# Performance work log

Measured on AMD Instinct MI355X. Metric: run time of the kernel, lower is better.

Reference implementation:

```python
import jax, jax.numpy as jnp
import numpy as np

SEQ_LEN, INPUT_DIM, HIDDEN_DIM, OUTPUT_DIM = 1024, 128, 256, 128
BATCH = 256


def setup_inputs() -> dict:
    key = jax.random.key(0)
    ks = jax.random.split(key, 7)
    s_ih = 1.0 / np.sqrt(INPUT_DIM)
    s_hh = 1.0 / np.sqrt(HIDDEN_DIM)
    return {
        "x": jax.random.normal(ks[0], (BATCH, SEQ_LEN, INPUT_DIM), jnp.float32),
        "W_ih": jax.random.normal(ks[1], (INPUT_DIM, 4 * HIDDEN_DIM), jnp.float32) * s_ih,
        "W_hh": jax.random.normal(ks[2], (HIDDEN_DIM, 4 * HIDDEN_DIM), jnp.float32) * s_hh,
        "b_ih": jax.random.normal(ks[3], (4 * HIDDEN_DIM,), jnp.float32) * s_hh,
        "b_hh": jax.random.normal(ks[4], (4 * HIDDEN_DIM,), jnp.float32) * s_hh,
        "W_out": jax.random.normal(ks[5], (HIDDEN_DIM, OUTPUT_DIM), jnp.float32) * s_hh,
        "b_out": jax.random.normal(ks[6], (OUTPUT_DIM,), jnp.float32) * s_hh,
    }


def reference(x, W_ih, W_hh, b_ih, b_hh, W_out, b_out):
    B, T, _ = x.shape
    H = W_hh.shape[0]
    # Precompute input projections for all timesteps: [T, B, 4H]
    x_proj = jnp.einsum("bti,ig->tbg", x, W_ih) + (b_ih + b_hh)

    def step(carry, xp_t):
        h, c = carry
        gates = xp_t + h @ W_hh  # [B, 4H]
        i_t, f_t, g_t, o_t = jnp.split(gates, 4, axis=1)
        i_t = jax.nn.sigmoid(i_t)
        f_t = jax.nn.sigmoid(f_t)
        g_t = jnp.tanh(g_t)
        o_t = jax.nn.sigmoid(o_t)
        c = f_t * c + i_t * g_t
        h = o_t * jnp.tanh(c)
        return (h, c), None

    h0 = jnp.zeros((B, H), x.dtype)
    c0 = jnp.zeros((B, H), x.dtype)
    (h_T, _), _ = jax.lax.scan(step, (h0, c0), x_proj)
    return h_T @ W_out + b_out
```

## Files before the change

kernel.cpp:

```cpp
#include <hip/hip_runtime.h>
#include <cstdint>


#define T_    1024
#define I_    128
#define H_    256

typedef short s8v __attribute__((ext_vector_type(8)));
typedef float f4v __attribute__((ext_vector_type(4)));
typedef unsigned short u16;
typedef unsigned int   u32;
typedef unsigned long long u64;

__device__ __forceinline__ u16 f2bf(float f) {
  union { float f; u32 u; } v; v.f = f;
  u32 r = v.u + 0x7FFFu + ((v.u >> 16) & 1u);
  return (u16)(r >> 16);
}
__device__ __forceinline__ float bf2f(u16 h) {
  union { u32 u; float f; } v; v.u = ((u32)h) << 16;
  return v.f;
}
__device__ __forceinline__ float sig_(float x)  { return 1.0f / (1.0f + __expf(-x)); }
__device__ __forceinline__ float tanh_(float x) { return 2.0f / (1.0f + __expf(-2.0f * x)) - 1.0f; }

__device__ __forceinline__ void unpack8(const u64 w[4], s8v& hi, s8v& lo) {
  #pragma unroll
  for (int j = 0; j < 4; j++) {
    u32 a = (u32)w[j], b = (u32)(w[j] >> 32);
    hi[2*j]   = (short)(u16)a;        lo[2*j]   = (short)(u16)(a >> 16);
    hi[2*j+1] = (short)(u16)b;        lo[2*j+1] = (short)(u16)(b >> 16);
  }
}

__global__ __launch_bounds__(256, 1) void lstm_persist(
    const float* __restrict__ x, const float* __restrict__ Wih,
    const float* __restrict__ Whh, const float* __restrict__ bih,
    const float* __restrict__ bhh, const float* __restrict__ Wout,
    const float* __restrict__ bout, float* __restrict__ out,
    u32* __restrict__ flags, u32* __restrict__ hbuf)
{
  const int bid  = blockIdx.x;
  const int xcd  = bid & 7;
  const int slot = bid >> 3;
  const int ct   = slot & 15;
  const int g    = ((slot >> 4) << 3) | xcd;
  const int tid  = threadIdx.x;
  const int wave = tid >> 6;
  const int lane = tid & 63;
  const int lm   = lane & 15;
  const int lq   = lane >> 4;

  __shared__ u16   Wlds[2][64][392];
  __shared__ u16   xlds[2][2][16][136];
  __shared__ float partial[4][4][16][20];

  for (int it = tid; it < 384 * 64; it += 256) {
    int k = it >> 6;
    int c = it & 63;
    int gcol = (c >> 4) * 256 + ct * 16 + (c & 15);
    float w = (k < 128) ? Wih[k * 1024 + gcol] : Whh[(k - 128) * 1024 + gcol];
    u16 hi = f2bf(w);
    Wlds[0][c][k] = hi;
    Wlds[1][c][k] = f2bf(w - bf2f(hi));
  }
  __syncthreads();

  s8v wfrag[3][4][2];
  #pragma unroll
  for (int ki = 0; ki < 3; ki++) {
    const int kt = wave + 4 * ki;
    #pragma unroll
    for (int gg = 0; gg < 4; gg++) {
      #pragma unroll
      for (int p = 0; p < 2; p++)
        wfrag[ki][gg][p] = *(const s8v*)&Wlds[p][gg * 16 + lm][kt * 32 + lq * 8];
    }
  }
  __syncthreads();

  const int cm  = tid >> 4;
  const int chc = tid & 15;
  float biasv[4];
  #pragma unroll
  for (int gg = 0; gg < 4; gg++) {
    int col = gg * 256 + ct * 16 + chc;
    biasv[gg] = bih[col] + bhh[col];
  }
  float cstate = 0.0f;

  const int xr  = tid >> 4;
  const int xc0 = (tid & 15) * 8;
  const float* xbase = x + (size_t)(g * 16 + xr) * (T_ * I_) + xc0;

  u32* gflags = flags + g * 32;
  const size_t hpar   = (size_t)16 * 16 * 256;
  const size_t hgbase = (size_t)g * 16 * 256;

  const int pl   = lane & 3;
  u32* fpeer = gflags + (2 * wave + (pl & 1) + 8 * (pl >> 1));

  auto xstore = [&](int par, float4 a, float4 b) {
    float v[8] = {a.x, a.y, a.z, a.w, b.x, b.y, b.z, b.w};
    union { u16 u[8]; s8v s; } hi, lo;
    #pragma unroll
    for (int j = 0; j < 8; j++) {
      u16 h = f2bf(v[j]);
      hi.u[j] = h;
      lo.u[j] = f2bf(v[j] - bf2f(h));
    }
    *(s8v*)&xlds[par][0][xr][xc0] = hi.s;
    *(s8v*)&xlds[par][1][xr][xc0] = lo.s;
  };

  {
    float4 a = *(const float4*)(xbase + 0);
    float4 b = *(const float4*)(xbase + 4);
    xstore(0, a, b);
  }
  __syncthreads();

  for (int t = 0; t < T_; t++) {
    const int par = t & 1;
    const int pn  = (t + 1) & 1;

    const int tn = (t + 1 < T_) ? (t + 1) : t;
    float4 xa = *(const float4*)(xbase + (size_t)tn * I_);
    float4 xb = *(const float4*)(xbase + (size_t)tn * I_ + 4);

    f4v acc[4];
    #pragma unroll
    for (int gg = 0; gg < 4; gg++)
      #pragma unroll
      for (int r = 0; r < 4; r++) acc[gg][r] = 0.0f;

    {
      s8v axh = *(const s8v*)&xlds[par][0][lm][wave * 32 + lq * 8];
      s8v axl = *(const s8v*)&xlds[par][1][lm][wave * 32 + lq * 8];
      #pragma unroll
      for (int gg = 0; gg < 4; gg++) {
        acc[gg] = __builtin_amdgcn_mfma_f32_16x16x32_bf16(axh, wfrag[0][gg][0], acc[gg], 0, 0, 0);
        acc[gg] = __builtin_amdgcn_mfma_f32_16x16x32_bf16(axl, wfrag[0][gg][0], acc[gg], 0, 0, 0);
        acc[gg] = __builtin_amdgcn_mfma_f32_16x16x32_bf16(axh, wfrag[0][gg][1], acc[gg], 0, 0, 0);
      }
    }

    if (t > 0) {
      const u32 s = (u32)t;
      while (true) {
        u32 f = __hip_atomic_load(fpeer, __ATOMIC_RELAXED, __HIP_MEMORY_SCOPE_AGENT);
        if (__all((int)((f - s) <= 1u))) break;
        __builtin_amdgcn_s_sleep(1);
      }
      asm volatile("" ::: "memory");

      const u32* hb0 = hbuf + (size_t)par * hpar + hgbase;
      #pragma unroll
      for (int ki = 1; ki < 3; ki++) {
        const int hk = wave * 32 + (ki - 1) * 128 + lq * 8;
        const u64* hp = (const u64*)(hb0 + (size_t)lm * 256 + hk);
        u64 w[4];
        #pragma unroll
        for (int j = 0; j < 4; j++)
          w[j] = __hip_atomic_load(hp + j, __ATOMIC_RELAXED, __HIP_MEMORY_SCOPE_AGENT);
        s8v ahh, ahl;
        unpack8(w, ahh, ahl);
        #pragma unroll
        for (int gg = 0; gg < 4; gg++) {
          acc[gg] = __builtin_amdgcn_mfma_f32_16x16x32_bf16(ahh, wfrag[ki][gg][0], acc[gg], 0, 0, 0);
          acc[gg] = __builtin_amdgcn_mfma_f32_16x16x32_bf16(ahl, wfrag[ki][gg][0], acc[gg], 0, 0, 0);
          acc[gg] = __builtin_amdgcn_mfma_f32_16x16x32_bf16(ahh, wfrag[ki][gg][1], acc[gg], 0, 0, 0);
        }
      }
    }

    #pragma unroll
    for (int gg = 0; gg < 4; gg++)
      #pragma unroll
      for (int r = 0; r < 4; r++)
        partial[wave][gg][lq * 4 + r][lm] = acc[gg][r];
    __syncthreads();

    float ga = biasv[0], gb = biasv[1], gc = biasv[2], gd = biasv[3];
    #pragma unroll
    for (int w = 0; w < 4; w++) {
      ga += partial[w][0][cm][chc];
      gb += partial[w][1][cm][chc];
      gc += partial[w][2][cm][chc];
      gd += partial[w][3][cm][chc];
    }
    float i_t = sig_(ga), f_t = sig_(gb), g_t = tanh_(gc), o_t = sig_(gd);
    cstate = f_t * cstate + i_t * g_t;
    float h = o_t * tanh_(cstate);

    u16 hhi = f2bf(h);
    u16 hlo = f2bf(h - bf2f(hhi));
    u32 pk  = ((u32)hlo << 16) | (u32)hhi;
    u32* hw = hbuf + (size_t)pn * hpar + hgbase + (size_t)cm * 256 + ct * 16 + chc;
    __hip_atomic_store(hw, pk, __ATOMIC_RELAXED, __HIP_MEMORY_SCOPE_AGENT);

    __syncthreads();
    if (tid == 0)
      __hip_atomic_store(gflags + ct, (u32)(t + 1), __ATOMIC_RELAXED, __HIP_MEMORY_SCOPE_AGENT);

    xstore(pn, xa, xb);
    __syncthreads();
  }

  {
    const u32 s = (u32)T_;
    u32* fp = gflags + lm;
    while (true) {
      u32 f = __hip_atomic_load(fp, __ATOMIC_RELAXED, __HIP_MEMORY_SCOPE_AGENT);
      if (__all((int)((f - s) <= 1u))) break;
      __builtin_amdgcn_s_sleep(1);
    }
    asm volatile("" ::: "memory");
  }
  __syncthreads();
  for (int it = tid; it < 16 * 256; it += 256) {
    int n = it >> 8;
    int k = it & 255;
    float w = (n < 8) ? Wout[k * 128 + ct * 8 + n] : 0.0f;
    u16 hi = f2bf(w);
    Wlds[0][n][k] = hi;
    Wlds[1][n][k] = f2bf(w - bf2f(hi));
  }
  __syncthreads();

  f4v oacc;
  #pragma unroll
  for (int r = 0; r < 4; r++) oacc[r] = 0.0f;
  const u32* hb0 = hbuf + hgbase;
  #pragma unroll
  for (int ki = 0; ki < 2; ki++) {
    const int hk = (wave * 2 + ki) * 32 + lq * 8;
    const u64* hp = (const u64*)(hb0 + (size_t)lm * 256 + hk);
    u64 w[4];
    #pragma unroll
    for (int j = 0; j < 4; j++)
      w[j] = __hip_atomic_load(hp + j, __ATOMIC_RELAXED, __HIP_MEMORY_SCOPE_AGENT);
    s8v ahh, ahl;
    unpack8(w, ahh, ahl);
    s8v bh  = *(const s8v*)&Wlds[0][lm][hk];
    s8v bl  = *(const s8v*)&Wlds[1][lm][hk];
    oacc = __builtin_amdgcn_mfma_f32_16x16x32_bf16(ahh, bh, oacc, 0, 0, 0);
    oacc = __builtin_amdgcn_mfma_f32_16x16x32_bf16(ahl, bh, oacc, 0, 0, 0);
    oacc = __builtin_amdgcn_mfma_f32_16x16x32_bf16(ahh, bl, oacc, 0, 0, 0);
  }
  #pragma unroll
  for (int r = 0; r < 4; r++) partial[wave][0][lq * 4 + r][lm] = oacc[r];
  __syncthreads();

  if (tid < 128) {
    int m  = tid >> 3;
    int oc = tid & 7;
    float v = bout[ct * 8 + oc];
    #pragma unroll
    for (int w = 0; w < 4; w++) v += partial[w][0][m][oc];
    out[(size_t)(g * 16 + m) * 128 + ct * 8 + oc] = v;
  }
}

extern "C" void kernel_launch(void* const* d_in, const int* in_sizes, int n_in,
                              void* d_out, int out_size, void* d_ws, size_t ws_size,
                              hipStream_t stream) {
  const float* x    = (const float*)d_in[0];
  const float* Wih  = (const float*)d_in[1];
  const float* Whh  = (const float*)d_in[2];
  const float* bih  = (const float*)d_in[3];
  const float* bhh  = (const float*)d_in[4];
  const float* Wout = (const float*)d_in[5];
  const float* bout = (const float*)d_in[6];
  float* out = (float*)d_out;

  char* ws = (char*)d_ws;
  u32* flags = (u32*)ws;
  u32* hbuf  = (u32*)(ws + 4096);

  hipLaunchKernelGGL(lstm_persist, dim3(256), dim3(256), 0, stream,
                     x, Wih, Whh, bih, bhh, Wout, bout, out, flags, hbuf);
}
```

Baseline: 3.151 ms.

## Replace per-block step flags with timestep-tagged 64-bit hidden-state words

Drops the separate flag array and the extra barrier plus flag store after each step. Each hidden value is now written as a 64-bit word whose upper half holds the step number, and consumers spin directly on the data until every tag matches. This removes one synchronisation round trip per timestep. In exchange it doubles the hidden-buffer traffic, busy-polls without sleeping, and leaves some dead unpack code.

```diff
diff --git a/kernel.cpp b/kernel.cpp
--- a/kernel.cpp
+++ b/kernel.cpp
@@ -24,12 +24,13 @@
 __device__ __forceinline__ float sig_(float x)  { return 1.0f / (1.0f + __expf(-x)); }
 __device__ __forceinline__ float tanh_(float x) { return 2.0f / (1.0f + __expf(-2.0f * x)) - 1.0f; }
 
-__device__ __forceinline__ void unpack8(const u64 w[4], s8v& hi, s8v& lo) {
+__device__ __forceinline__ void unpack4(const u64 w[4], s8v& hi, s8v& lo) {
   #pragma unroll
   for (int j = 0; j < 4; j++) {
-    u32 a = (u32)w[j], b = (u32)(w[j] >> 32);
-    hi[2*j]   = (short)(u16)a;        lo[2*j]   = (short)(u16)(a >> 16);
-    hi[2*j+1] = (short)(u16)b;        lo[2*j+1] = (short)(u16)(b >> 16);
+    u32 d = (u32)w[j];
+    hi[2*j]   = (short)(u16)d;
+    lo[2*j]   = (short)(u16)(d >> 16);
+    (void)0;
   }
 }
 
@@ -38,7 +39,7 @@
     const float* __restrict__ Whh, const float* __restrict__ bih,
     const float* __restrict__ bhh, const float* __restrict__ Wout,
     const float* __restrict__ bout, float* __restrict__ out,
-    u32* __restrict__ flags, u32* __restrict__ hbuf)
+    u64* __restrict__ hbuf)
 {
   const int bid  = blockIdx.x;
   const int xcd  = bid & 7;
@@ -93,12 +94,8 @@
   const int xc0 = (tid & 15) * 8;
   const float* xbase = x + (size_t)(g * 16 + xr) * (T_ * I_) + xc0;
 
-  u32* gflags = flags + g * 32;
   const size_t hpar   = (size_t)16 * 16 * 256;
   const size_t hgbase = (size_t)g * 16 * 256;
-
-  const int pl   = lane & 3;
-  u32* fpeer = gflags + (2 * wave + (pl & 1) + 8 * (pl >> 1));
 
   auto xstore = [&](int par, float4 a, float4 b) {
     float v[8] = {a.x, a.y, a.z, a.w, b.x, b.y, b.z, b.w};
@@ -119,6 +116,8 @@
     xstore(0, a, b);
   }
   __syncthreads();
+
+  const size_t hoff = (size_t)lm * 256 + wave * 32 + lq * 8;
 
   for (int t = 0; t < T_; t++) {
     const int par = t & 1;
@@ -146,30 +145,75 @@
     }
 
     if (t > 0) {
+      const u64* hp = hbuf + (size_t)par * hpar + hgbase + hoff;
       const u32 s = (u32)t;
+      u64 w0[4], w1[4];
       while (true) {
-        u32 f = __hip_atomic_load(fpeer, __ATOMIC_RELAXED, __HIP_MEMORY_SCOPE_AGENT);
-        if (__all((int)((f - s) <= 1u))) break;
-        __builtin_amdgcn_s_sleep(1);
+        #pragma unroll
+        for (int j = 0; j < 4; j++) {
+          w0[j] = __hip_atomic_load(hp + j,       __ATOMIC_RELAXED, __HIP_MEMORY_SCOPE_AGENT);
+          w1[j] = __hip_atomic_load(hp + 128 + j, __ATOMIC_RELAXED, __HIP_MEMORY_SCOPE_AGENT);
+        }
+        bool ok = true;
+        #pragma unroll
+        for (int j = 0; j < 4; j++)
+          ok &= ((u32)(w0[j] >> 32) == s) & ((u32)(w1[j] >> 32) == s);
+        if (__all(ok)) break;
       }
-      asm volatile("" ::: "memory");
-
-      const u32* hb0 = hbuf + (size_t)par * hpar + hgbase;
+
       #pragma unroll
       for (int ki = 1; ki < 3; ki++) {
-        const int hk = wave * 32 + (ki - 1) * 128 + lq * 8;
-        const u64* hp = (const u64*)(hb0 + (size_t)lm * 256 + hk);
-        u64 w[4];
-        #pragma unroll
-        for (int j = 0; j < 4; j++)
-          w[j] = __hip_atomic_load(hp + j, __ATOMIC_RELAXED, __HIP_MEMORY_SCOPE_AGENT);
+        const u64* w = (ki == 1) ? w0 : w1;
         s8v ahh, ahl;
-        unpack8(w, ahh, ahl);
+        #pragma unroll
+        for (int j = 0; j < 4; j++) {
+          u32 d = (u32)w[j];
+          ahh[j] = 0; ahl[j] = 0; (void)d;
+        }
+        (void)ahh; (void)ahl;
+      }
+      {
+        const u64* hp2 = hp + 4;
+        u64 w0b[4], w1b[4];
+        #pragma unroll
+        for (int j = 0; j < 4; j++) {
+          w0b[j] = __hip_atomic_load(hp2 + j,       __ATOMIC_RELAXED, __HIP_MEMORY_SCOPE_AGENT);
+          w1b[j] = __hip_atomic_load(hp2 + 128 + j, __ATOMIC_RELAXED, __HIP_MEMORY_SCOPE_AGENT);
+        }
+        bool ok2;
+        do {
+          ok2 = true;
+          #pragma unroll
+          for (int j = 0; j < 4; j++)
+            ok2 &= ((u32)(w0b[j] >> 32) == (u32)t) & ((u32)(w1b[j] >> 32) == (u32)t);
+          if (!__all(ok2)) {
+            #pragma unroll
+            for (int j = 0; j < 4; j++) {
+              w0b[j] = __hip_atomic_load(hp2 + j,       __ATOMIC_RELAXED, __HIP_MEMORY_SCOPE_AGENT);
+              w1b[j] = __hip_atomic_load(hp2 + 128 + j, __ATOMIC_RELAXED, __HIP_MEMORY_SCOPE_AGENT);
+            }
+            ok2 = false;
+          }
+        } while (!__all(ok2));
+
+        s8v ahh1, ahl1, ahh2, ahl2;
+        #pragma unroll
+        for (int j = 0; j < 4; j++) {
+          u32 d0 = (u32)w0[j], d0b = (u32)w0b[j];
+          u32 d1 = (u32)w1[j], d1b = (u32)w1b[j];
+          ahh1[j]     = (short)(u16)d0;          ahl1[j]     = (short)(u16)(d0 >> 16);
+          ahh1[j + 4] = (short)(u16)d0b;         ahl1[j + 4] = (short)(u16)(d0b >> 16);
+          ahh2[j]     = (short)(u16)d1;          ahl2[j]     = (short)(u16)(d1 >> 16);
+          ahh2[j + 4] = (short)(u16)d1b;         ahl2[j + 4] = (short)(u16)(d1b >> 16);
+        }
         #pragma unroll
         for (int gg = 0; gg < 4; gg++) {
-          acc[gg] = __builtin_amdgcn_mfma_f32_16x16x32_bf16(ahh, wfrag[ki][gg][0], acc[gg], 0, 0, 0);
-          acc[gg] = __builtin_amdgcn_mfma_f32_16x16x32_bf16(ahl, wfrag[ki][gg][0], acc[gg], 0, 0, 0);
-          acc[gg] = __builtin_amdgcn_mfma_f32_16x16x32_bf16(ahh, wfrag[ki][gg][1], acc[gg], 0, 0, 0);
+          acc[gg] = __builtin_amdgcn_mfma_f32_16x16x32_bf16(ahh1, wfrag[1][gg][0], acc[gg], 0, 0, 0);
+          acc[gg] = __builtin_amdgcn_mfma_f32_16x16x32_bf16(ahl1, wfrag[1][gg][0], acc[gg], 0, 0, 0);
+          acc[gg] = __builtin_amdgcn_mfma_f32_16x16x32_bf16(ahh1, wfrag[1][gg][1], acc[gg], 0, 0, 0);
+          acc[gg] = __builtin_amdgcn_mfma_f32_16x16x32_bf16(ahh2, wfrag[2][gg][0], acc[gg], 0, 0, 0);
+          acc[gg] = __builtin_amdgcn_mfma_f32_16x16x32_bf16(ahl2, wfrag[2][gg][0], acc[gg], 0, 0, 0);
+          acc[gg] = __builtin_amdgcn_mfma_f32_16x16x32_bf16(ahh2, wfrag[2][gg][1], acc[gg], 0, 0, 0);
         }
       }
     }
@@ -195,29 +239,14 @@
 
     u16 hhi = f2bf(h);
     u16 hlo = f2bf(h - bf2f(hhi));
-    u32 pk  = ((u32)hlo << 16) | (u32)hhi;
-    u32* hw = hbuf + (size_t)pn * hpar + hgbase + (size_t)cm * 256 + ct * 16 + chc;
-    __hip_atomic_store(hw, pk, __ATOMIC_RELAXED, __HIP_MEMORY_SCOPE_AGENT);
-
-    __syncthreads();
-    if (tid == 0)
-      __hip_atomic_store(gflags + ct, (u32)(t + 1), __ATOMIC_RELAXED, __HIP_MEMORY_SCOPE_AGENT);
+    u64 val = ((u64)(u32)(t + 1) << 32) | ((u32)hlo << 16) | (u32)hhi;
+    u64* hw = hbuf + (size_t)pn * hpar + hgbase + (size_t)cm * 256 + ct * 16 + chc;
+    __hip_atomic_store(hw, val, __ATOMIC_RELAXED, __HIP_MEMORY_SCOPE_AGENT);
 
     xstore(pn, xa, xb);
     __syncthreads();
   }
 
-  {
-    const u32 s = (u32)T_;
-    u32* fp = gflags + lm;
-    while (true) {
-      u32 f = __hip_atomic_load(fp, __ATOMIC_RELAXED, __HIP_MEMORY_SCOPE_AGENT);
-      if (__all((int)((f - s) <= 1u))) break;
-      __builtin_amdgcn_s_sleep(1);
-    }
-    asm volatile("" ::: "memory");
-  }
-  __syncthreads();
   for (int it = tid; it < 16 * 256; it += 256) {
     int n = it >> 8;
     int k = it & 255;
@@ -231,17 +260,28 @@
   f4v oacc;
   #pragma unroll
   for (int r = 0; r < 4; r++) oacc[r] = 0.0f;
-  const u32* hb0 = hbuf + hgbase;
+  const u64* hb0 = hbuf + hgbase;
   #pragma unroll
   for (int ki = 0; ki < 2; ki++) {
     const int hk = (wave * 2 + ki) * 32 + lq * 8;
-    const u64* hp = (const u64*)(hb0 + (size_t)lm * 256 + hk);
-    u64 w[4];
-    #pragma unroll
-    for (int j = 0; j < 4; j++)
-      w[j] = __hip_atomic_load(hp + j, __ATOMIC_RELAXED, __HIP_MEMORY_SCOPE_AGENT);
+    const u64* hp = hb0 + (size_t)lm * 256 + hk;
+    u64 w[8];
+    bool ok;
+    do {
+      #pragma unroll
+      for (int j = 0; j < 8; j++)
+        w[j] = __hip_atomic_load(hp + j, __ATOMIC_RELAXED, __HIP_MEMORY_SCOPE_AGENT);
+      ok = true;
+      #pragma unroll
+      for (int j = 0; j < 8; j++) ok &= ((u32)(w[j] >> 32) == (u32)T_);
+    } while (!__all(ok));
     s8v ahh, ahl;
-    unpack8(w, ahh, ahl);
+    #pragma unroll
+    for (int j = 0; j < 8; j++) {
+      u32 d = (u32)w[j];
+      ahh[j] = (short)(u16)d;
+      ahl[j] = (short)(u16)(d >> 16);
+    }
     s8v bh  = *(const s8v*)&Wlds[0][lm][hk];
     s8v bl  = *(const s8v*)&Wlds[1][lm][hk];
     oacc = __builtin_amdgcn_mfma_f32_16x16x32_bf16(ahh, bh, oacc, 0, 0, 0);
@@ -274,10 +314,8 @@
   const float* bout = (const float*)d_in[6];
   float* out = (float*)d_out;
 
-  char* ws = (char*)d_ws;
-  u32* flags = (u32*)ws;
-  u32* hbuf  = (u32*)(ws + 4096);
+  u64* hbuf = (u64*)d_ws;
 
   hipLaunchKernelGGL(lstm_persist, dim3(256), dim3(256), 0, stream,
-                     x, Wih, Whh, bih, bhh, Wout, bout, out, flags, hbuf);
-}
+                     x, Wih, Whh, bih, bhh, Wout, bout, out, hbuf);
+}
```

After: 3.624 ms. 15.0% more time.
